# Kernel optimization log

Measured on AMD Instinct MI355X. Metric: run time of the kernel, lower is better.

Reference implementation:

```python
import jax, jax.numpy as jnp
import numpy as np

B, T, D, H, L, C = 64, 256, 128, 1024, 5, 10


def setup_inputs() -> dict:
    key = jax.random.key(0)
    ks = jax.random.split(key, 6)
    def init(k, shape, fan_in):
        return jax.random.normal(k, shape, jnp.float32) / np.float32(np.sqrt(fan_in))
    x = jax.random.normal(ks[0], (B, T, D), jnp.float32)
    Wx0 = init(ks[1], (D, 4 * H), D)            # layer 0 input weights
    Wxs = init(ks[2], (L - 1, H, 4 * H), H)     # layers 1..L-1 input weights
    Whs = init(ks[3], (L, H, 4 * H), H)         # recurrent weights
    bs = jnp.zeros((L, 4 * H), jnp.float32)     # gate biases
    W_head = init(ks[4], (H, C), H)
    b_head = jnp.zeros((C,), jnp.float32)
    return {"x": x, "Wx0": Wx0, "Wxs": Wxs, "Whs": Whs, "bs": bs,
            "W_head": W_head, "b_head": b_head}


def _lstm_layer(xs, Wx, Wh, b):
    # xs: [T, B, in_d] time-major; returns hidden sequence [T, B, H]
    Bsz = xs.shape[1]
    Hd = Wh.shape[0]
    def step(carry, x_t):
        c, h = carry
        z = x_t @ Wx + h @ Wh + b            # [B, 4H], gate order i,f,g,o (flax)
        i, f, g, o = jnp.split(z, 4, axis=-1)
        c_new = jax.nn.sigmoid(f) * c + jax.nn.sigmoid(i) * jnp.tanh(g)
        h_new = jax.nn.sigmoid(o) * jnp.tanh(c_new)
        return (c_new, h_new), h_new
    init = (jnp.zeros((Bsz, Hd), xs.dtype), jnp.zeros((Bsz, Hd), xs.dtype))
    _, hs = jax.lax.scan(step, init, xs)
    return hs


def reference(x, Wx0, Wxs, Whs, bs, W_head, b_head):
    xs = jnp.swapaxes(x, 0, 1)                  # [T, B, D]
    xs = _lstm_layer(xs, Wx0, Whs[0], bs[0])
    for l in range(1, L):
        xs = _lstm_layer(xs, Wxs[l - 1], Whs[l], bs[l])
    return xs[-1] @ W_head + b_head             # [B, C] from last timestep
```

## Files before the change

kernel.cpp:

```cpp
#include <hip/hip_runtime.h>
#include <hip/hip_cooperative_groups.h>
#include <hip/hip_bf16.h>
#include <cstddef>

typedef unsigned short u16;
typedef unsigned long long u64t;
typedef __attribute__((ext_vector_type(8))) short s8;
typedef __attribute__((ext_vector_type(4))) float f4;

constexpr int kB = 64, kT = 256, kD = 128, kH = 1024, kL = 5, kC = 10, kG = 4096;
constexpr int BH = kB * kH;
constexpr size_t WLA_ELEMS = (size_t)256 * 8 * 16384;
constexpr size_t WLB_ELEMS = (size_t)256 * 8 * 2560;
constexpr size_t H2_ELEMS = (size_t)kL * kT * BH;
constexpr int NBLK = 256;


__device__ __forceinline__ float sigf(float x) { return 1.f / (1.f + __expf(-x)); }
__device__ __forceinline__ float tanh_s(float x) {
  float ax = fabsf(x);
  float e = __expf(-2.f * ax);
  float r = (1.f - e) / (1.f + e);
  return copysignf(r, x);
}
__device__ __forceinline__ void split_bf16(float v, short& hi, short& lo) {
  __hip_bfloat16 h = __float2bfloat16(v);
  hi = __builtin_bit_cast(short, h);
  float fh = __bfloat162float(h);
  __hip_bfloat16 l = __float2bfloat16(v - fh);
  lo = __builtin_bit_cast(short, l);
}
__device__ __forceinline__ short hi_bf16(float v) {
  __hip_bfloat16 h = __float2bfloat16(v);
  return __builtin_bit_cast(short, h);
}
__device__ __forceinline__ float bf2f(u16 v) {
  unsigned u = ((unsigned)v) << 16;
  return __builtin_bit_cast(float, u);
}

__device__ __forceinline__ void sth8(u16* p, u64t v) {
  __hip_atomic_store((u64t*)p, v, __ATOMIC_RELAXED, __HIP_MEMORY_SCOPE_AGENT);
}

__device__ __forceinline__ void dma16(const void* gsrc, void* ldst) {
  __builtin_amdgcn_global_load_lds(
      (const __attribute__((address_space(1))) void*)gsrc,
      (__attribute__((address_space(3))) void*)ldst, 16, 0, 0);
}

__global__ void __launch_bounds__(512) split_wl(const float* __restrict__ Wx0,
                                                const float* __restrict__ Wxs,
                                                const float* __restrict__ Whs,
                                                u16* __restrict__ wlA,
                                                u16* __restrict__ wlB,
                                                unsigned* __restrict__ bar) {
  const int g = blockIdx.x, tid = threadIdx.x;
  const int wv = tid >> 6, lane = tid & 63, quad = lane >> 4, r = lane & 15;
  const int lA = (g >> 6) + 1, jb = g & 63, kq = wv & 3, ch = wv >> 2;
  const float* WxA = Wxs + (size_t)(lA - 1) * kH * kG;
  const float* WhA = Whs + (size_t)lA * kH * kG;

  if (g == 0 && tid < 512) bar[tid] = 0;

  u16* dA = wlA + (size_t)(g * 8 + wv) * 16384;
  for (int p = 0; p < 16; ++p) {
    int kc = 4 * p + kq;
    const float* W = (kc < 32) ? WxA : WhA;
    int krow0 = (kc & 31) * 32 + quad * 8;
    for (int ntl = 0; ntl < 2; ++ntl) {
      int col = (2 * ch + ntl) * kH + jb * 16 + r;
      s8 l8;
      for (int j = 0; j < 8; ++j) {
        float w = W[(size_t)(krow0 + j) * kG + col];
        short hh, ll;
        split_bf16(w, hh, ll);
        l8[j] = ll;
      }
      *(s8*)(dA + (size_t)((p * 2 + ntl) * 64 + lane) * 8) = l8;
    }
  }

  u16* dB = wlB + (size_t)(g * 8 + wv) * 2560;
  int colB = (r >> 2) * kH + g * 4 + (r & 3);
  for (int j2 = 0; j2 < 4; ++j2) {
    int kb = (wv & 3) + 4 * (2 * j2 + (wv >> 2));
    int krow0 = kb * 32 + quad * 8;
    s8 l8;
    for (int j = 0; j < 8; ++j) {
      float w = Whs[(size_t)(krow0 + j) * kG + colB];
      short hh, ll;
      split_bf16(w, hh, ll);
      l8[j] = ll;
    }
    *(s8*)(dB + (size_t)(j2 * 64 + lane) * 8) = l8;
  }
  {
    int krow0 = (wv & 3) * 32 + quad * 8;
    s8 l8;
    for (int j = 0; j < 8; ++j) {
      float w = Wx0[(size_t)(krow0 + j) * kG + colB];
      short hh, ll;
      split_bf16(w, hh, ll);
      l8[j] = ll;
    }
    *(s8*)(dB + (size_t)(4 * 64 + lane) * 8) = l8;
  }
}

__global__ void __launch_bounds__(512, 2) lstm_persist(
    const float* __restrict__ x, const float* __restrict__ Wx0,
    const float* __restrict__ Wxs, const float* __restrict__ Whs,
    const float* __restrict__ bs, const float* __restrict__ W_head,
    const float* __restrict__ b_head, float* __restrict__ out,
    u16* __restrict__ hhi, u16* __restrict__ hlo,
    const u16* __restrict__ wlA, const u16* __restrict__ wlB,
    unsigned* __restrict__ bar) {
  __shared__ s8 wpark[8][4][2][64];
  __shared__ s8 wring[8][4][2][64];
  __shared__ float zA[64 * 66];
  __shared__ float zB[64 * 18];
  __shared__ u16 hstA[2][128][8];
  __shared__ u16 hstB[2][64][4];

  const int tid = threadIdx.x;
  const int wv = tid >> 6, lane = tid & 63, quad = lane >> 4, r = lane & 15;
  const int ch = wv >> 2, kq = wv & 3;
  const int g = blockIdx.x;
  const int lA = (g >> 6) + 1;
  const int jb = g & 63;
  const int ub = g * 4;

  const float* __restrict__ WxA = Wxs + (size_t)(lA - 1) * kH * kG;
  const float* __restrict__ WhA = Whs + (size_t)lA * kH * kG;

  s8 wA[16][2];
#pragma unroll
  for (int p = 0; p < 16; ++p) {
    int kc = 4 * p + kq;
    const float* W = (kc < 32) ? WxA : WhA;
    int krow0 = (kc & 31) * 32 + quad * 8;
#pragma unroll
    for (int ntl = 0; ntl < 2; ++ntl) {
      int col = (2 * ch + ntl) * kH + jb * 16 + r;
      s8 h8;
#pragma unroll
      for (int j = 0; j < 8; ++j) h8[j] = hi_bf16(W[(size_t)(krow0 + j) * kG + col]);
      wA[p][ntl] = h8;
    }
  }
  s8 wBh[4], wBx;
  {
    int colB = (r >> 2) * kH + ub + (r & 3);
#pragma unroll
    for (int j2 = 0; j2 < 4; ++j2) {
      int kb = (wv & 3) + 4 * (2 * j2 + (wv >> 2));
      int krow0 = kb * 32 + quad * 8;
      s8 h8;
#pragma unroll
      for (int j = 0; j < 8; ++j) h8[j] = hi_bf16(Whs[(size_t)(krow0 + j) * kG + colB]);
      wBh[j2] = h8;
    }
    int krow0 = (wv & 3) * 32 + quad * 8;
    s8 h8;
#pragma unroll
    for (int j = 0; j < 8; ++j) h8[j] = hi_bf16(Wx0[(size_t)(krow0 + j) * kG + colB]);
    wBx = h8;
  }

  const u16* wlAs = wlA + (size_t)(g * 8 + wv) * 16384;
  const u16* wlBs = wlB + (size_t)(g * 8 + wv) * 2560;

#pragma unroll
  for (int p = 0; p < 4; ++p)
#pragma unroll
    for (int ntl = 0; ntl < 2; ++ntl)
      wpark[wv][p][ntl][lane] =
          *(const s8*)(wlAs + (size_t)((p * 2 + ntl) * 64 + lane) * 8);

  float bA[4], bB[4];
  {
    int u = tid & 15;
#pragma unroll
    for (int g4 = 0; g4 < 4; ++g4) bA[g4] = bs[(size_t)lA * kG + g4 * kH + jb * 16 + u];
    int u2 = tid & 3;
#pragma unroll
    for (int g4 = 0; g4 < 4; ++g4) bB[g4] = bs[(size_t)g4 * kH + ub + u2];
  }
  float cA0 = 0.f, cA1 = 0.f, cB0 = 0.f;
  const s8 zf = {0, 0, 0, 0, 0, 0, 0, 0};
  const f4 zero4 = {0.f, 0.f, 0.f, 0.f};
  const int fragbase = kq * 4 + quad;

  __syncthreads();

  for (int s = 0; s < kT + kL - 1; ++s) {
    const int tA = s - lA;
    const int tB = s;

    for (int i = tid; i < 64 * 66; i += 512) zA[i] = 0.f;
    for (int i = tid; i < 64 * 18; i += 512) zB[i] = 0.f;
    __syncthreads();

    if (tA >= 0 && tA < kT) {
      const int tAm1 = (tA > 0) ? tA - 1 : 0;
      const u16* IH = hhi + ((size_t)(lA - 1) * kT + tA) * BH;
      const u16* IL = hlo + ((size_t)(lA - 1) * kT + tA) * BH;
      const u16* RH = hhi + ((size_t)lA * kT + tAm1) * BH;
      const u16* RL = hlo + ((size_t)lA * kT + tAm1) * BH;
      const bool zz = (tA == 0);
      f4 accA[2][4];
#pragma unroll
      for (int a = 0; a < 2; ++a)
#pragma unroll
        for (int b = 0; b < 4; ++b) accA[a][b] = zero4;

#pragma unroll
      for (int c = 4; c <= 5; ++c)
#pragma unroll
        for (int ntl = 0; ntl < 2; ++ntl)
          dma16(wlAs + (size_t)((c * 2 + ntl) * 64 + lane) * 8,
                &wring[wv][c & 3][ntl][0]);
      s8 ah_n[4], al_n[4];
#pragma unroll
      for (int mt = 0; mt < 4; ++mt) {
        ah_n[mt] = *(const s8*)(IH + (size_t)(fragbase * 64 + mt * 16 + r) * 8);
        al_n[mt] = *(const s8*)(IL + (size_t)(fragbase * 64 + mt * 16 + r) * 8);
      }

#pragma unroll
      for (int p = 0; p < 16; ++p) {
        const bool curR = (p >= 8);
        __builtin_amdgcn_sched_barrier(0);
        if (p >= 4) {
          asm volatile("s_waitcnt vmcnt(4)" ::: "memory");
          __builtin_amdgcn_sched_barrier(0);
        }
        s8 wl0, wl1;
        if (p < 4) {
          wl0 = wpark[wv][p][0][lane];
          wl1 = wpark[wv][p][1][lane];
        } else {
          wl0 = wring[wv][p & 3][0][lane];
          wl1 = wring[wv][p & 3][1][lane];
        }
        s8 ah_c[4], al_c[4];
#pragma unroll
        for (int mt = 0; mt < 4; ++mt) {
          ah_c[mt] = (curR && zz) ? zf : ah_n[mt];
          al_c[mt] = (curR && zz) ? zf : al_n[mt];
        }
        if (p < 15) {
          const int pn = p + 1;
          const u16* SH = (pn >= 8) ? RH : IH;
          const u16* SL = (pn >= 8) ? RL : IL;
          const int kb8 = ((pn & 7) * 16 + fragbase) * 64;
#pragma unroll
          for (int mt = 0; mt < 4; ++mt) {
            ah_n[mt] = *(const s8*)(SH + (size_t)(kb8 + mt * 16 + r) * 8);
            al_n[mt] = *(const s8*)(SL + (size_t)(kb8 + mt * 16 + r) * 8);
          }
        }
        if (p >= 3 && p <= 12) {
          const int c = p + 3;
#pragma unroll
          for (int ntl = 0; ntl < 2; ++ntl)
            dma16(wlAs + (size_t)((c * 2 + ntl) * 64 + lane) * 8,
                  &wring[wv][c & 3][ntl][0]);
        }
#pragma unroll
        for (int mt = 0; mt < 4; ++mt) {
          f4 a0 = accA[0][mt], a1 = accA[1][mt];
          a0 = __builtin_amdgcn_mfma_f32_16x16x32_bf16(ah_c[mt], wA[p][0], a0, 0, 0, 0);
          a0 = __builtin_amdgcn_mfma_f32_16x16x32_bf16(al_c[mt], wA[p][0], a0, 0, 0, 0);
          a0 = __builtin_amdgcn_mfma_f32_16x16x32_bf16(ah_c[mt], wl0, a0, 0, 0, 0);
          a1 = __builtin_amdgcn_mfma_f32_16x16x32_bf16(ah_c[mt], wA[p][1], a1, 0, 0, 0);
          a1 = __builtin_amdgcn_mfma_f32_16x16x32_bf16(al_c[mt], wA[p][1], a1, 0, 0, 0);
          a1 = __builtin_amdgcn_mfma_f32_16x16x32_bf16(ah_c[mt], wl1, a1, 0, 0, 0);
          accA[0][mt] = a0;
          accA[1][mt] = a1;
        }
      }
#pragma unroll
      for (int ntl = 0; ntl < 2; ++ntl)
#pragma unroll
        for (int mt = 0; mt < 4; ++mt)
#pragma unroll
          for (int v = 0; v < 4; ++v)
            atomicAdd(&zA[(mt * 16 + quad * 4 + v) * 66 + (2 * ch + ntl) * 16 + r],
                      accA[ntl][mt][v]);
    }

    if (tB < kT) {
      const int tBm1 = (tB > 0) ? tB - 1 : 0;
      const u16* H0H = hhi + (size_t)tBm1 * BH;
      const u16* H0L = hlo + (size_t)tBm1 * BH;
      const bool z0 = (tB == 0);
      f4 accB[4];
#pragma unroll
      for (int b = 0; b < 4; ++b) accB[b] = zero4;

      s8 wlb_n = *(const s8*)(wlBs + (size_t)(0 * 64 + lane) * 8);
      s8 ahb_n[4];
      {
        const int kb0 = (wv & 3) + 4 * (wv >> 2);
        const int kb8 = (kb0 * 4 + quad) * 64;
#pragma unroll
        for (int mt = 0; mt < 4; ++mt)
          ahb_n[mt] = *(const s8*)(H0H + (size_t)(kb8 + mt * 16 + r) * 8);
      }
#pragma unroll
      for (int j2 = 0; j2 < 4; ++j2) {
        const int kb = (wv & 3) + 4 * (2 * j2 + (wv >> 2));
        const int kb8c = (kb * 4 + quad) * 64;
        s8 wlv = wlb_n;
        s8 ahb_c[4];
#pragma unroll
        for (int mt = 0; mt < 4; ++mt) ahb_c[mt] = z0 ? zf : ahb_n[mt];
        if (j2 < 3) {
          wlb_n = *(const s8*)(wlBs + (size_t)((j2 + 1) * 64 + lane) * 8);
          const int kbn = (wv & 3) + 4 * (2 * (j2 + 1) + (wv >> 2));
          const int kb8n = (kbn * 4 + quad) * 64;
#pragma unroll
          for (int mt = 0; mt < 4; ++mt)
            ahb_n[mt] = *(const s8*)(H0H + (size_t)(kb8n + mt * 16 + r) * 8);
        }
        s8 alb[4];
#pragma unroll
        for (int mt = 0; mt < 4; ++mt) {
          s8 v = *(const s8*)(H0L + (size_t)(kb8c + mt * 16 + r) * 8);
          alb[mt] = z0 ? zf : v;
        }
#pragma unroll
        for (int mt = 0; mt < 4; ++mt) {
          f4 a = accB[mt];
          a = __builtin_amdgcn_mfma_f32_16x16x32_bf16(ahb_c[mt], wBh[j2], a, 0, 0, 0);
          a = __builtin_amdgcn_mfma_f32_16x16x32_bf16(alb[mt], wBh[j2], a, 0, 0, 0);
          a = __builtin_amdgcn_mfma_f32_16x16x32_bf16(ahb_c[mt], wlv, a, 0, 0, 0);
          accB[mt] = a;
        }
      }
      if (wv >= 4) {
        const int c = wv - 4;
        s8 wlx = *(const s8*)(wlBs + (size_t)(4 * 64 + lane) * 8);
#pragma unroll
        for (int mt = 0; mt < 4; ++mt) {
          const float* sx =
              x + (size_t)(mt * 16 + r) * kT * kD + (size_t)tB * kD + c * 32 + quad * 8;
          float4 v0 = *(const float4*)sx;
          float4 v1 = *(const float4*)(sx + 4);
          float vv[8] = {v0.x, v0.y, v0.z, v0.w, v1.x, v1.y, v1.z, v1.w};
          s8 xh, xl;
#pragma unroll
          for (int e = 0; e < 8; ++e) {
            short hh, ll;
            split_bf16(vv[e], hh, ll);
            xh[e] = hh;
            xl[e] = ll;
          }
          f4 a = accB[mt];
          a = __builtin_amdgcn_mfma_f32_16x16x32_bf16(xh, wBx, a, 0, 0, 0);
          a = __builtin_amdgcn_mfma_f32_16x16x32_bf16(xl, wBx, a, 0, 0, 0);
          a = __builtin_amdgcn_mfma_f32_16x16x32_bf16(xh, wlx, a, 0, 0, 0);
          accB[mt] = a;
        }
      }
#pragma unroll
      for (int mt = 0; mt < 4; ++mt)
#pragma unroll
        for (int v = 0; v < 4; ++v)
          atomicAdd(&zB[(mt * 16 + quad * 4 + v) * 18 + r], accB[mt][v]);
    }

    __syncthreads();

    if (tA >= 0 && tA < kT) {
#pragma unroll
      for (int rp = 0; rp < 2; ++rp) {
        int p2 = tid + 512 * rp;
        int b = p2 >> 4, u = p2 & 15;
        float zi = zA[b * 66 + u] + bA[0];
        float zfg = zA[b * 66 + 16 + u] + bA[1];
        float zg = zA[b * 66 + 32 + u] + bA[2];
        float zo = zA[b * 66 + 48 + u] + bA[3];
        float cp = (tA == 0) ? 0.f : (rp ? cA1 : cA0);
        float cn = sigf(zfg) * cp + sigf(zi) * tanh_s(zg);
        float hn = sigf(zo) * tanh_s(cn);
        if (rp) cA1 = cn; else cA0 = cn;
        short hh, ll;
        split_bf16(hn, hh, ll);
        hstA[0][(u >> 3) * 64 + b][u & 7] = (u16)hh;
        hstA[1][(u >> 3) * 64 + b][u & 7] = (u16)ll;
      }
    }
    if (tB < kT && tid < 256) {
      int b = tid >> 2, u2 = tid & 3;
      float zi = zB[b * 18 + u2] + bB[0];
      float zfg = zB[b * 18 + 4 + u2] + bB[1];
      float zg = zB[b * 18 + 8 + u2] + bB[2];
      float zo = zB[b * 18 + 12 + u2] + bB[3];
      float cp = (tB == 0) ? 0.f : cB0;
      float cn = sigf(zfg) * cp + sigf(zi) * tanh_s(zg);
      float hn = sigf(zo) * tanh_s(cn);
      cB0 = cn;
      short hh, ll;
      split_bf16(hn, hh, ll);
      hstB[0][b][u2] = (u16)hh;
      hstB[1][b][u2] = (u16)ll;
    }
    __syncthreads();

    if (tA >= 0 && tA < kT) {
      u16* HA = ((wv < 4) ? hhi : hlo) + ((size_t)lA * kT + tA) * BH;
      const int arr = wv >> 2;
      const int ci = (wv & 3) * 64 + lane;
      const int gi = ci >> 1, half = ci & 1;
      u64t v = *(const u64t*)&hstA[arr][gi][half * 4];
      sth8(HA + ((size_t)(jb * 2 + (gi >> 6)) * 64 + (gi & 63)) * 8 + half * 4, v);
    }
    if (tB < kT && wv < 2) {
      u16* HB = (wv ? hlo : hhi) + (size_t)tB * BH;
      u64t v = *(const u64t*)&hstB[wv][lane][0];
      sth8(HB + ((size_t)(ub >> 3) * 64 + lane) * 8 + (ub & 7), v);
    }

    asm volatile("s_waitcnt vmcnt(0) lgkmcnt(0)" ::: "memory");
    __syncthreads();
    if (tid == 0) {
      __hip_atomic_fetch_add(&bar[s], 1u, __ATOMIC_RELAXED, __HIP_MEMORY_SCOPE_AGENT);
      while (__hip_atomic_load(&bar[s], __ATOMIC_RELAXED, __HIP_MEMORY_SCOPE_AGENT) <
             (unsigned)NBLK)
        __builtin_amdgcn_s_sleep(1);
    }
    __syncthreads();
    asm volatile("" ::: "memory");
  }

  if (g < 80) {
    int p = g * 8 + wv;
    int b = p / 10, cc = p - b * 10;
    const u16* HH = hhi + ((size_t)kL * kT - 1) * BH;
    const u16* HL = hlo + ((size_t)kL * kT - 1) * BH;
    float sum = 0.f;
    for (int j = lane; j < kH; j += 64) {
      size_t off = ((size_t)(j >> 3) * 64 + b) * 8 + (j & 7);
      sum += (bf2f(HH[off]) + bf2f(HL[off])) * W_head[(size_t)j * kC + cc];
    }
#pragma unroll
    for (int off = 32; off > 0; off >>= 1) sum += __shfl_down(sum, off, 64);
    if (lane == 0) out[p] = sum + b_head[cc];
  }
}

static u16* g_wl = nullptr;
__attribute__((constructor)) static void alloc_wl() {
  hipMalloc((void**)&g_wl,
            (WLA_ELEMS + WLB_ELEMS + 2 * H2_ELEMS) * sizeof(u16) + 4096);
}

extern "C" void kernel_launch(void* const* d_in, const int* in_sizes, int n_in,
                              void* d_out, int out_size, void* d_ws, size_t ws_size,
                              hipStream_t stream) {
  const float* x = (const float*)d_in[0];
  const float* Wx0 = (const float*)d_in[1];
  const float* Wxs = (const float*)d_in[2];
  const float* Whs = (const float*)d_in[3];
  const float* bs = (const float*)d_in[4];
  const float* W_head = (const float*)d_in[5];
  const float* b_head = (const float*)d_in[6];
  float* out = (float*)d_out;

  size_t need = (2 * H2_ELEMS + WLA_ELEMS + WLB_ELEMS) * sizeof(u16) + 4096;
  u16* base = (ws_size >= need) ? (u16*)d_ws : g_wl;
  u16* hhi = base;
  u16* hlo = hhi + H2_ELEMS;
  u16* wlA = hlo + H2_ELEMS;
  u16* wlB = wlA + WLA_ELEMS;
  unsigned* bar = (unsigned*)(wlB + WLB_ELEMS);

  split_wl<<<256, 512, 0, stream>>>(Wx0, Wxs, Whs, wlA, wlB, bar);

  void* args[] = {&x, &Wx0, &Wxs, &Whs, &bs, &W_head, &b_head,
                  &out, &hhi, &hlo, &wlA, &wlB, &bar};
  hipLaunchCooperativeKernel((void*)lstm_persist, dim3(256), dim3(512), args, 0,
                             stream);
}
```

Baseline: 20.58 ms.

## Use hierarchical tree grid barrier and deepen layer-A operand prefetch pipeline

The flat global atomic barrier, where all 256 blocks increment and poll one counter every step, becomes a two-level tree. Blocks arrive at 16 leaf counters, leaf leaders combine at a root counter, then release their leaf through a per-leaf flag. This aims to cut atomic contention and polling traffic on a single cache line. The layer-A MFMA loop is also restructured: hi activation fragments are prefetched two steps ahead, the weight DMA ring depth goes from 2 to 4 in flight, lo fragments load just in time, and the low-precision MFMAs are issued separately with explicit vmcnt waits. The hand-tuned waitcnt values are fragile, and the tree adds extra barrier latency hops.

```diff
diff --git a/kernel.cpp b/kernel.cpp
--- a/kernel.cpp
+++ b/kernel.cpp
@@ -13,7 +13,6 @@
 constexpr size_t WLA_ELEMS = (size_t)256 * 8 * 16384;
 constexpr size_t WLB_ELEMS = (size_t)256 * 8 * 2560;
 constexpr size_t H2_ELEMS = (size_t)kL * kT * BH;
-constexpr int NBLK = 256;
 
 
 __device__ __forceinline__ float sigf(float x) { return 1.f / (1.f + __expf(-x)); }
@@ -41,6 +40,9 @@
 
 __device__ __forceinline__ void sth8(u16* p, u64t v) {
   __hip_atomic_store((u64t*)p, v, __ATOMIC_RELAXED, __HIP_MEMORY_SCOPE_AGENT);
+}
+__device__ __forceinline__ unsigned aload(const unsigned* p) {
+  return __hip_atomic_load(p, __ATOMIC_RELAXED, __HIP_MEMORY_SCOPE_AGENT);
 }
 
 __device__ __forceinline__ void dma16(const void* gsrc, void* ldst) {
@@ -61,7 +63,8 @@
   const float* WxA = Wxs + (size_t)(lA - 1) * kH * kG;
   const float* WhA = Whs + (size_t)lA * kH * kG;
 
-  if (g == 0 && tid < 512) bar[tid] = 0;
+  if (g == 0)
+    for (int i = tid; i < 2048; i += 512) bar[i] = 0;
 
   u16* dA = wlA + (size_t)(g * 8 + wv) * 16384;
   for (int p = 0; p < 16; ++p) {
@@ -216,26 +219,34 @@
         for (int b = 0; b < 4; ++b) accA[a][b] = zero4;
 
 #pragma unroll
-      for (int c = 4; c <= 5; ++c)
+      for (int c = 4; c <= 7; ++c)
 #pragma unroll
         for (int ntl = 0; ntl < 2; ++ntl)
           dma16(wlAs + (size_t)((c * 2 + ntl) * 64 + lane) * 8,
                 &wring[wv][c & 3][ntl][0]);
-      s8 ah_n[4], al_n[4];
-#pragma unroll
-      for (int mt = 0; mt < 4; ++mt) {
-        ah_n[mt] = *(const s8*)(IH + (size_t)(fragbase * 64 + mt * 16 + r) * 8);
-        al_n[mt] = *(const s8*)(IL + (size_t)(fragbase * 64 + mt * 16 + r) * 8);
-      }
+      s8 ah_sl[2][4];
+#pragma unroll
+      for (int pp = 0; pp < 2; ++pp)
+#pragma unroll
+        for (int mt = 0; mt < 4; ++mt)
+          ah_sl[pp][mt] =
+              *(const s8*)(IH + (size_t)((pp * 16 + fragbase) * 64 + mt * 16 + r) * 8);
 
 #pragma unroll
       for (int p = 0; p < 16; ++p) {
         const bool curR = (p >= 8);
         __builtin_amdgcn_sched_barrier(0);
-        if (p >= 4) {
-          asm volatile("s_waitcnt vmcnt(4)" ::: "memory");
-          __builtin_amdgcn_sched_barrier(0);
-        }
+        const u16* SL = curR ? RL : IL;
+        const int kb8c = ((p & 7) * 16 + fragbase) * 64;
+        s8 al_c[4];
+#pragma unroll
+        for (int mt = 0; mt < 4; ++mt)
+          al_c[mt] = *(const s8*)(SL + (size_t)(kb8c + mt * 16 + r) * 8);
+        if (p == 15)      asm volatile("s_waitcnt vmcnt(20)" ::: "memory");
+        else if (p == 14) asm volatile("s_waitcnt vmcnt(26)" ::: "memory");
+        else if (p == 13) asm volatile("s_waitcnt vmcnt(28)" ::: "memory");
+        else              asm volatile("s_waitcnt vmcnt(30)" ::: "memory");
+        __builtin_amdgcn_sched_barrier(0);
         s8 wl0, wl1;
         if (p < 4) {
           wl0 = wpark[wv][p][0][lane];
@@ -244,41 +255,43 @@
           wl0 = wring[wv][p & 3][0][lane];
           wl1 = wring[wv][p & 3][1][lane];
         }
-        s8 ah_c[4], al_c[4];
+        s8 ah_c[4];
+#pragma unroll
+        for (int mt = 0; mt < 4; ++mt) ah_c[mt] = (curR && zz) ? zf : ah_sl[p & 1][mt];
 #pragma unroll
         for (int mt = 0; mt < 4; ++mt) {
-          ah_c[mt] = (curR && zz) ? zf : ah_n[mt];
-          al_c[mt] = (curR && zz) ? zf : al_n[mt];
-        }
-        if (p < 15) {
-          const int pn = p + 1;
+          f4 a0 = accA[0][mt], a1 = accA[1][mt];
+          a0 = __builtin_amdgcn_mfma_f32_16x16x32_bf16(ah_c[mt], wA[p][0], a0, 0, 0, 0);
+          a0 = __builtin_amdgcn_mfma_f32_16x16x32_bf16(ah_c[mt], wl0, a0, 0, 0, 0);
+          a1 = __builtin_amdgcn_mfma_f32_16x16x32_bf16(ah_c[mt], wA[p][1], a1, 0, 0, 0);
+          a1 = __builtin_amdgcn_mfma_f32_16x16x32_bf16(ah_c[mt], wl1, a1, 0, 0, 0);
+          accA[0][mt] = a0;
+          accA[1][mt] = a1;
+        }
+        if (p < 14) {
+          const int pn = p + 2;
           const u16* SH = (pn >= 8) ? RH : IH;
-          const u16* SL = (pn >= 8) ? RL : IL;
-          const int kb8 = ((pn & 7) * 16 + fragbase) * 64;
-#pragma unroll
-          for (int mt = 0; mt < 4; ++mt) {
-            ah_n[mt] = *(const s8*)(SH + (size_t)(kb8 + mt * 16 + r) * 8);
-            al_n[mt] = *(const s8*)(SL + (size_t)(kb8 + mt * 16 + r) * 8);
-          }
-        }
-        if (p >= 3 && p <= 12) {
-          const int c = p + 3;
+          const int kb8n = ((pn & 7) * 16 + fragbase) * 64;
+#pragma unroll
+          for (int mt = 0; mt < 4; ++mt)
+            ah_sl[p & 1][mt] = *(const s8*)(SH + (size_t)(kb8n + mt * 16 + r) * 8);
+        }
+        if (p >= 4 && p <= 11) {
+          const int c = p + 4;
 #pragma unroll
           for (int ntl = 0; ntl < 2; ++ntl)
             dma16(wlAs + (size_t)((c * 2 + ntl) * 64 + lane) * 8,
                   &wring[wv][c & 3][ntl][0]);
         }
+        s8 alz[4];
+#pragma unroll
+        for (int mt = 0; mt < 4; ++mt) alz[mt] = (curR && zz) ? zf : al_c[mt];
 #pragma unroll
         for (int mt = 0; mt < 4; ++mt) {
-          f4 a0 = accA[0][mt], a1 = accA[1][mt];
-          a0 = __builtin_amdgcn_mfma_f32_16x16x32_bf16(ah_c[mt], wA[p][0], a0, 0, 0, 0);
-          a0 = __builtin_amdgcn_mfma_f32_16x16x32_bf16(al_c[mt], wA[p][0], a0, 0, 0, 0);
-          a0 = __builtin_amdgcn_mfma_f32_16x16x32_bf16(ah_c[mt], wl0, a0, 0, 0, 0);
-          a1 = __builtin_amdgcn_mfma_f32_16x16x32_bf16(ah_c[mt], wA[p][1], a1, 0, 0, 0);
-          a1 = __builtin_amdgcn_mfma_f32_16x16x32_bf16(al_c[mt], wA[p][1], a1, 0, 0, 0);
-          a1 = __builtin_amdgcn_mfma_f32_16x16x32_bf16(ah_c[mt], wl1, a1, 0, 0, 0);
-          accA[0][mt] = a0;
-          accA[1][mt] = a1;
+          accA[0][mt] =
+              __builtin_amdgcn_mfma_f32_16x16x32_bf16(alz[mt], wA[p][0], accA[0][mt], 0, 0, 0);
+          accA[1][mt] =
+              __builtin_amdgcn_mfma_f32_16x16x32_bf16(alz[mt], wA[p][1], accA[1][mt], 0, 0, 0);
         }
       }
 #pragma unroll
@@ -427,10 +440,21 @@
     asm volatile("s_waitcnt vmcnt(0) lgkmcnt(0)" ::: "memory");
     __syncthreads();
     if (tid == 0) {
-      __hip_atomic_fetch_add(&bar[s], 1u, __ATOMIC_RELAXED, __HIP_MEMORY_SCOPE_AGENT);
-      while (__hip_atomic_load(&bar[s], __ATOMIC_RELAXED, __HIP_MEMORY_SCOPE_AGENT) <
-             (unsigned)NBLK)
-        __builtin_amdgcn_s_sleep(1);
+      const int leaf = g >> 4;
+      const unsigned tgt = 16u * (unsigned)(s + 1);
+      __hip_atomic_fetch_add(&bar[leaf * 32], 1u, __ATOMIC_RELAXED,
+                             __HIP_MEMORY_SCOPE_AGENT);
+      if ((g & 15) == 0) {
+        while (aload(&bar[leaf * 32]) < tgt) __builtin_amdgcn_s_sleep(1);
+        __hip_atomic_fetch_add(&bar[512], 1u, __ATOMIC_RELAXED,
+                               __HIP_MEMORY_SCOPE_AGENT);
+        while (aload(&bar[512]) < tgt) __builtin_amdgcn_s_sleep(2);
+        __hip_atomic_store(&bar[544 + leaf * 32], (unsigned)(s + 1),
+                           __ATOMIC_RELAXED, __HIP_MEMORY_SCOPE_AGENT);
+      } else {
+        while (aload(&bar[544 + leaf * 32]) < (unsigned)(s + 1))
+          __builtin_amdgcn_s_sleep(4);
+      }
     }
     __syncthreads();
     asm volatile("" ::: "memory");
@@ -455,7 +479,7 @@
 static u16* g_wl = nullptr;
 __attribute__((constructor)) static void alloc_wl() {
   hipMalloc((void**)&g_wl,
-            (WLA_ELEMS + WLB_ELEMS + 2 * H2_ELEMS) * sizeof(u16) + 4096);
+            (WLA_ELEMS + WLB_ELEMS + 2 * H2_ELEMS) * sizeof(u16) + 16384);
 }
 
 extern "C" void kernel_launch(void* const* d_in, const int* in_sizes, int n_in,
@@ -470,7 +494,7 @@
   const float* b_head = (const float*)d_in[6];
   float* out = (float*)d_out;
 
-  size_t need = (2 * H2_ELEMS + WLA_ELEMS + WLB_ELEMS) * sizeof(u16) + 4096;
+  size_t need = (2 * H2_ELEMS + WLA_ELEMS + WLB_ELEMS) * sizeof(u16) + 16384;
   u16* base = (ws_size >= need) ? (u16*)d_ws : g_wl;
   u16* hhi = base;
   u16* hlo = hhi + H2_ELEMS;
```

Result: no change. 20.36 ms (-1.1%).
